# Kernel tuning notes

Hardware: AMD Instinct MI355X
Metric: run time of the kernel (lower is better)

## Reference

```python
import jax, jax.numpy as jnp
import numpy as np

N, E = 50000, 800000
DIN, DH, DOUT = 128, 128, 64


def _w(k, fan_in, fan_out):
    return (jax.random.normal(k, (fan_in, fan_out), jnp.float32) / np.sqrt(fan_in)).astype(jnp.float32)


def setup_inputs() -> dict:
    key = jax.random.key(0)
    ks = jax.random.split(key, 12)
    x = jax.random.normal(ks[0], (N, DIN), jnp.float32)
    edge_index = jax.random.randint(ks[1], (2, E), 0, N, dtype=jnp.int64)
    return {
        "x": x,
        "edge_index": edge_index,
        # sage1 block: SAGEConv(DIN->DH) -> relu -> SAGEConv(DH->DH)
        "Ws11": _w(ks[2], DIN, DH), "Wn11": _w(ks[3], DIN, DH), "b11": jnp.zeros((DH,), jnp.float32),
        "Ws12": _w(ks[4], DH, DH),  "Wn12": _w(ks[5], DH, DH),  "b12": jnp.zeros((DH,), jnp.float32),
        # sage2 block: SAGEConv(DH->DH) -> relu -> SAGEConv(DH->DH)
        "Ws21": _w(ks[6], DH, DH),  "Wn21": _w(ks[7], DH, DH),  "b21": jnp.zeros((DH,), jnp.float32),
        "Ws22": _w(ks[8], DH, DH),  "Wn22": _w(ks[9], DH, DH),  "b22": jnp.zeros((DH,), jnp.float32),
        # classifier
        "Wc": _w(ks[10], DH, DOUT), "bc": jnp.zeros((DOUT,), jnp.float32),
    }


def _sage_conv(h, src, tgt, Ws, Wn, b, n):
    # mean-aggregate neighbor features (src -> tgt), then self + neighbor linear
    msgs = h[src]                                                   # [E, d] gather
    deg = jax.ops.segment_sum(jnp.ones((src.shape[0],), h.dtype), tgt, num_segments=n)
    agg = jax.ops.segment_sum(msgs, tgt, num_segments=n)
    agg = agg / jnp.maximum(deg, 1.0)[:, None]                      # [n, d]
    return h @ Ws + agg @ Wn + b


def reference(x, edge_index, Ws11, Wn11, b11, Ws12, Wn12, b12,
              Ws21, Wn21, b21, Ws22, Wn22, b22, Wc, bc):
    src, tgt = edge_index[0], edge_index[1]
    n = x.shape[0]
    # sage1 block (2 layers) + outer relu
    h = jax.nn.relu(_sage_conv(x, src, tgt, Ws11, Wn11, b11, n))
    h = _sage_conv(h, src, tgt, Ws12, Wn12, b12, n)
    h = jax.nn.relu(h)
    # dropout (eval mode): identity
    # sage2 block (2 layers) + outer relu
    h = jax.nn.relu(_sage_conv(h, src, tgt, Ws21, Wn21, b21, n))
    h = _sage_conv(h, src, tgt, Ws22, Wn22, b22, n)
    h = jax.nn.relu(h)
    # global mean pool over nodes, then classify
    g = jnp.mean(h, axis=0)                                         # [DH]
    return g @ Wc + bc                                              # [DOUT]
```

## Files before the change

kernel.cpp:

```cpp
#include <hip/hip_runtime.h>
#include <hip/hip_bf16.h>
#include <hip/hip_fp16.h>


typedef _Float16 f16x8 __attribute__((ext_vector_type(8)));
typedef float f32x4 __attribute__((ext_vector_type(4)));

__global__ __launch_bounds__(256) void k_bucket(
    const int* __restrict__ src, const int* __restrict__ tgt,
    int* __restrict__ deg, unsigned long long* __restrict__ staging,
    int* __restrict__ bucket_fill, int E, int bdiv, int cap) {
  __shared__ unsigned long long buf[8][320];
  __shared__ int cnt[8];
  __shared__ int base[8];
  int tid = threadIdx.x;
  int lane = tid & 63;
  if (tid < 8) cnt[tid] = 0;
  __syncthreads();
  int e0 = blockIdx.x * 2048;
#pragma unroll
  for (int i = 0; i < 8; ++i) {
    int e = e0 + i * 256 + tid;
    bool valid = e < E;
    int b = -1;
    unsigned long long pair = 0;
    if (valid) {
      int t = tgt[e];
      int s = src[e];
      atomicAdd(&deg[t], 1);
      b = t / bdiv;
      pair = ((unsigned long long)(unsigned)t << 32) | (unsigned)s;
    }
#pragma unroll
    for (int bk = 0; bk < 8; ++bk) {
      bool mine = (b == bk);
      unsigned long long mask = __ballot(mine);
      if (mask == 0ull) continue;
      int cw = __popcll(mask);
      int leader = __ffsll((unsigned long long)mask) - 1;
      int p0 = 0;
      if (lane == leader) p0 = atomicAdd(&cnt[bk], cw);
      p0 = __shfl(p0, leader, 64);
      if (mine) {
        int p = p0 + __popcll(mask & ((1ull << lane) - 1ull));
        if (p < 320) {
          buf[bk][p] = pair;
        } else {
          int gp = atomicAdd(&bucket_fill[bk], 1);
          staging[(size_t)bk * cap + gp] = pair;
        }
      }
    }
  }
  __syncthreads();
  if (tid < 8) {
    int c = min(cnt[tid], 320);
    base[tid] = atomicAdd(&bucket_fill[tid], c);
    cnt[tid] = c;
  }
  __syncthreads();
  for (int b = 0; b < 8; ++b) {
    int c = cnt[b];
    for (int p = tid; p < c; p += 256)
      staging[(size_t)b * cap + base[b] + p] = buf[b][p];
  }
}

__global__ __launch_bounds__(256) void k_scatter2(
    const unsigned long long* __restrict__ staging,
    const int* __restrict__ bucket_fill, int* __restrict__ cursor,
    int* __restrict__ csr_src, int cap) {
  int b = blockIdx.x & 7;
  int nchunk = gridDim.x >> 3;
  int chunk = blockIdx.x >> 3;
  int n = bucket_fill[b];
  const unsigned long long* sb = staging + (size_t)b * cap;
  for (int i0 = chunk * 2048; i0 < n; i0 += nchunk * 2048) {
#pragma unroll
    for (int t = 0; t < 8; ++t) {
      int i = i0 + t * 256 + (int)threadIdx.x;
      if (i < n) {
        unsigned long long pair = sb[i];
        int tg = (int)(pair >> 32);
        int s = (int)(pair & 0xffffffffu);
        int pos = atomicAdd(&cursor[tg], 1);
        csr_src[pos] = s;
      }
    }
  }
}

__global__ __launch_bounds__(256) void k_scan1(const int* __restrict__ deg,
                                               int* __restrict__ partial,
                                               int* __restrict__ blocksum,
                                               float* __restrict__ inv_deg, int n) {
  __shared__ int s[256];
  int tid = threadIdx.x;
  int i = blockIdx.x * 256 + tid;
  int v = (i < n) ? deg[i] : 0;
  s[tid] = v;
  __syncthreads();
  for (int off = 1; off < 256; off <<= 1) {
    int t = (tid >= off) ? s[tid - off] : 0;
    __syncthreads();
    s[tid] += t;
    __syncthreads();
  }
  if (i < n) {
    partial[i] = s[tid] - v;
    inv_deg[i] = 1.0f / fmaxf((float)v, 1.0f);
  }
  if (tid == 255) blocksum[blockIdx.x] = s[255];
}

__global__ __launch_bounds__(256) void k_scan2(int* __restrict__ blocksum, int nb) {
  __shared__ int s[256];
  int tid = threadIdx.x;
  int v = (tid < nb) ? blocksum[tid] : 0;
  s[tid] = v;
  __syncthreads();
  for (int off = 1; off < 256; off <<= 1) {
    int t = (tid >= off) ? s[tid - off] : 0;
    __syncthreads();
    s[tid] += t;
    __syncthreads();
  }
  if (tid < nb) blocksum[tid] = s[tid] - v;
}

__global__ __launch_bounds__(256) void k_scan3(const int* __restrict__ partial,
                                               const int* __restrict__ blocksum,
                                               int* __restrict__ row_start,
                                               int* __restrict__ cursor, int n, int E) {
  int i = blockIdx.x * 256 + threadIdx.x;
  if (i < n) {
    int r = partial[i] + blocksum[blockIdx.x];
    row_start[i] = r;
    cursor[i] = r;
  }
  if (i == 0) row_start[n] = E;
}

__global__ __launch_bounds__(256) void k_cvt_x(const float* __restrict__ x,
                                               __half* __restrict__ xh, int total8) {
  int i = blockIdx.x * 256 + threadIdx.x;
  if (i >= total8) return;
  const float4* p = (const float4*)(x + (size_t)i * 8);
  float4 v0 = p[0], v1 = p[1];
  f16x8 o;
  o[0] = (_Float16)v0.x; o[1] = (_Float16)v0.y; o[2] = (_Float16)v0.z; o[3] = (_Float16)v0.w;
  o[4] = (_Float16)v1.x; o[5] = (_Float16)v1.y; o[6] = (_Float16)v1.z; o[7] = (_Float16)v1.w;
  *(f16x8*)(xh + (size_t)i * 8) = o;
}

struct WPack {
  const float* s[4];
  const float* n[4];
};

__global__ __launch_bounds__(256) void k_prep_w(WPack p, __half* __restrict__ Wt) {
  int l = blockIdx.y;
  int i = blockIdx.x * 256 + threadIdx.x;
  int n = i >> 8;
  int k = i & 255;
  const float* W = (k < 128) ? p.s[l] : p.n[l];
  float v = W[(size_t)(k & 127) * 128 + n];
  Wt[(size_t)l * 32768 + (size_t)n * 256 + k] = __float2half(v);
}

__global__ __launch_bounds__(256) void k_agg_h(
    const __half* __restrict__ h, const int* __restrict__ csr_src,
    const int* __restrict__ row_start, const float* __restrict__ inv_deg,
    __half* __restrict__ agg, int n_nodes) {
  int gw = (blockIdx.x * 256 + (int)threadIdx.x) >> 6;
  int lane = threadIdx.x & 63;
  if (gw >= n_nodes) return;
  int q = lane >> 4;
  int dl = (lane & 15) * 8;
  int beg = row_start[gw];
  int end = row_start[gw + 1];
  float a0 = 0.f, a1 = 0.f, a2 = 0.f, a3 = 0.f;
  float a4 = 0.f, a5 = 0.f, a6 = 0.f, a7 = 0.f;
  int e = beg;
  for (; e + 16 <= end; e += 16) {
    int i0 = csr_src[e + q];
    int i1 = csr_src[e + 4 + q];
    int i2 = csr_src[e + 8 + q];
    int i3 = csr_src[e + 12 + q];
    f16x8 v0 = *(const f16x8*)(h + (size_t)i0 * 128 + dl);
    f16x8 v1 = *(const f16x8*)(h + (size_t)i1 * 128 + dl);
    f16x8 v2 = *(const f16x8*)(h + (size_t)i2 * 128 + dl);
    f16x8 v3 = *(const f16x8*)(h + (size_t)i3 * 128 + dl);
    a0 += ((float)v0[0] + (float)v1[0]) + ((float)v2[0] + (float)v3[0]);
    a1 += ((float)v0[1] + (float)v1[1]) + ((float)v2[1] + (float)v3[1]);
    a2 += ((float)v0[2] + (float)v1[2]) + ((float)v2[2] + (float)v3[2]);
    a3 += ((float)v0[3] + (float)v1[3]) + ((float)v2[3] + (float)v3[3]);
    a4 += ((float)v0[4] + (float)v1[4]) + ((float)v2[4] + (float)v3[4]);
    a5 += ((float)v0[5] + (float)v1[5]) + ((float)v2[5] + (float)v3[5]);
    a6 += ((float)v0[6] + (float)v1[6]) + ((float)v2[6] + (float)v3[6]);
    a7 += ((float)v0[7] + (float)v1[7]) + ((float)v2[7] + (float)v3[7]);
  }
  for (; e + 8 <= end; e += 8) {
    int i0 = csr_src[e + q];
    int i1 = csr_src[e + 4 + q];
    f16x8 v0 = *(const f16x8*)(h + (size_t)i0 * 128 + dl);
    f16x8 v1 = *(const f16x8*)(h + (size_t)i1 * 128 + dl);
    a0 += (float)v0[0] + (float)v1[0];
    a1 += (float)v0[1] + (float)v1[1];
    a2 += (float)v0[2] + (float)v1[2];
    a3 += (float)v0[3] + (float)v1[3];
    a4 += (float)v0[4] + (float)v1[4];
    a5 += (float)v0[5] + (float)v1[5];
    a6 += (float)v0[6] + (float)v1[6];
    a7 += (float)v0[7] + (float)v1[7];
  }
  for (; e + 4 <= end; e += 4) {
    int i0 = csr_src[e + q];
    f16x8 v0 = *(const f16x8*)(h + (size_t)i0 * 128 + dl);
    a0 += (float)v0[0];
    a1 += (float)v0[1];
    a2 += (float)v0[2];
    a3 += (float)v0[3];
    a4 += (float)v0[4];
    a5 += (float)v0[5];
    a6 += (float)v0[6];
    a7 += (float)v0[7];
  }
  if (e + q < end) {
    int i0 = csr_src[e + q];
    f16x8 v0 = *(const f16x8*)(h + (size_t)i0 * 128 + dl);
    a0 += (float)v0[0];
    a1 += (float)v0[1];
    a2 += (float)v0[2];
    a3 += (float)v0[3];
    a4 += (float)v0[4];
    a5 += (float)v0[5];
    a6 += (float)v0[6];
    a7 += (float)v0[7];
  }
  a0 += __shfl_xor(a0, 16, 64);
  a1 += __shfl_xor(a1, 16, 64);
  a2 += __shfl_xor(a2, 16, 64);
  a3 += __shfl_xor(a3, 16, 64);
  a4 += __shfl_xor(a4, 16, 64);
  a5 += __shfl_xor(a5, 16, 64);
  a6 += __shfl_xor(a6, 16, 64);
  a7 += __shfl_xor(a7, 16, 64);
  a0 += __shfl_xor(a0, 32, 64);
  a1 += __shfl_xor(a1, 32, 64);
  a2 += __shfl_xor(a2, 32, 64);
  a3 += __shfl_xor(a3, 32, 64);
  a4 += __shfl_xor(a4, 32, 64);
  a5 += __shfl_xor(a5, 32, 64);
  a6 += __shfl_xor(a6, 32, 64);
  a7 += __shfl_xor(a7, 32, 64);
  if (q == 0) {
    float wgt = inv_deg[gw];
    f16x8 r;
    r[0] = (_Float16)(a0 * wgt);
    r[1] = (_Float16)(a1 * wgt);
    r[2] = (_Float16)(a2 * wgt);
    r[3] = (_Float16)(a3 * wgt);
    r[4] = (_Float16)(a4 * wgt);
    r[5] = (_Float16)(a5 * wgt);
    r[6] = (_Float16)(a6 * wgt);
    r[7] = (_Float16)(a7 * wgt);
    *(f16x8*)(agg + (size_t)gw * 128 + dl) = r;
  }
}

__global__ __launch_bounds__(256) void k_linear_mfma(
    const __half* __restrict__ h, const __half* __restrict__ agg,
    const __half* __restrict__ Wt, const float* __restrict__ bias,
    __half* __restrict__ out, int n_nodes) {
  int tid = threadIdx.x;
  int cq = tid >> 6;
  int lane = tid & 63;
  int node0 = blockIdx.x * 64;
  int lr = lane & 15;
  int lg = lane >> 4;

  f32x4 acc[4][2];
#pragma unroll
  for (int rt = 0; rt < 4; ++rt)
#pragma unroll
    for (int ct = 0; ct < 2; ++ct) acc[rt][ct] = (f32x4){0.f, 0.f, 0.f, 0.f};

  const __half* hrow[4];
  const __half* grow[4];
#pragma unroll
  for (int rt = 0; rt < 4; ++rt) {
    int arow = node0 + rt * 16 + lr;
    if (arow >= n_nodes) arow = n_nodes - 1;
    hrow[rt] = h + (size_t)arow * 128;
    grow[rt] = agg + (size_t)arow * 128;
  }

#pragma unroll
  for (int ks = 0; ks < 8; ++ks) {
    int koff = (ks & 3) * 32 + lg * 8;
    int kb = ks * 32 + lg * 8;
    f16x8 b0 = *(const f16x8*)(Wt + (size_t)(cq * 32 + lr) * 256 + kb);
    f16x8 b1 = *(const f16x8*)(Wt + (size_t)(cq * 32 + 16 + lr) * 256 + kb);
#pragma unroll
    for (int rt = 0; rt < 4; ++rt) {
      f16x8 a = (ks < 4) ? *(const f16x8*)(hrow[rt] + koff)
                         : *(const f16x8*)(grow[rt] + koff);
      acc[rt][0] = __builtin_amdgcn_mfma_f32_16x16x32_f16(a, b0, acc[rt][0], 0, 0, 0);
      acc[rt][1] = __builtin_amdgcn_mfma_f32_16x16x32_f16(a, b1, acc[rt][1], 0, 0, 0);
    }
  }

#pragma unroll
  for (int ct = 0; ct < 2; ++ct) {
    int n_col = cq * 32 + ct * 16 + lr;
    float bv = bias[n_col];
#pragma unroll
    for (int rt = 0; rt < 4; ++rt) {
#pragma unroll
      for (int r = 0; r < 4; ++r) {
        int m = node0 + rt * 16 + lg * 4 + r;
        if (m < n_nodes)
          out[(size_t)m * 128 + n_col] = __float2half(fmaxf(acc[rt][ct][r] + bv, 0.f));
      }
    }
  }
}

__global__ __launch_bounds__(256) void k_pool(const __half* __restrict__ h,
                                              float* __restrict__ partial, int n_nodes) {
  __shared__ float red[4][128];
  int tid = threadIdx.x;
  int lane = tid & 63;
  int w = tid >> 6;
  float a0 = 0.f, a1 = 0.f;
  for (int n = blockIdx.x * 4 + w; n < n_nodes; n += gridDim.x * 4) {
    float2 f = __half22float2(*(const __half2*)(h + (size_t)n * 128 + lane * 2));
    a0 += f.x;
    a1 += f.y;
  }
  red[w][lane * 2] = a0;
  red[w][lane * 2 + 1] = a1;
  __syncthreads();
  if (tid < 128) {
    partial[(size_t)blockIdx.x * 128 + tid] =
        (red[0][tid] + red[1][tid]) + (red[2][tid] + red[3][tid]);
  }
}

__global__ __launch_bounds__(512) void k_final(const float* __restrict__ partial,
                                               const float* __restrict__ Wc,
                                               const float* __restrict__ bc,
                                               float* __restrict__ out, int n_nodes) {
  __shared__ float red[4][128];
  __shared__ float gs[128];
  __shared__ float red2[8][64];
  int tid = threadIdx.x;
  int j = tid & 127;
  int c = tid >> 7;
  float s = 0.f;
#pragma unroll
  for (int b = 0; b < 64; ++b) s += partial[(size_t)(c * 64 + b) * 128 + j];
  red[c][j] = s;
  __syncthreads();
  if (tid < 128) {
    float g = (red[0][tid] + red[1][tid]) + (red[2][tid] + red[3][tid]);
    gs[tid] = g / (float)n_nodes;
  }
  __syncthreads();
  {
    int jo = tid & 63;
    int c2 = tid >> 6;
    float s2 = 0.f;
#pragma unroll
    for (int d = 0; d < 16; ++d)
      s2 += gs[c2 * 16 + d] * Wc[(size_t)(c2 * 16 + d) * 64 + jo];
    red2[c2][jo] = s2;
  }
  __syncthreads();
  if (tid < 64) {
    float o = bc[tid];
#pragma unroll
    for (int c2 = 0; c2 < 8; ++c2) o += red2[c2][tid];
    out[tid] = o;
  }
}

extern "C" void kernel_launch(void* const* d_in, const int* in_sizes, int n_in,
                              void* d_out, int out_size, void* d_ws, size_t ws_size,
                              hipStream_t stream) {
  const float* x = (const float*)d_in[0];
  const int* ei = (const int*)d_in[1];
  const float* Ws11 = (const float*)d_in[2];
  const float* Wn11 = (const float*)d_in[3];
  const float* b11 = (const float*)d_in[4];
  const float* Ws12 = (const float*)d_in[5];
  const float* Wn12 = (const float*)d_in[6];
  const float* b12 = (const float*)d_in[7];
  const float* Ws21 = (const float*)d_in[8];
  const float* Wn21 = (const float*)d_in[9];
  const float* b21 = (const float*)d_in[10];
  const float* Ws22 = (const float*)d_in[11];
  const float* Wn22 = (const float*)d_in[12];
  const float* b22 = (const float*)d_in[13];
  const float* Wc = (const float*)d_in[14];
  const float* bc = (const float*)d_in[15];

  int N = in_sizes[0] / 128;
  int E = in_sizes[1] / 2;
  const int* src = ei;
  const int* tgt = ei + E;

  int bdiv = (N + 7) / 8;
  int cap = E / 8 + 8192;

  char* w = (char*)d_ws;
  size_t off = 0;
  auto alloc = [&](size_t bytes) {
    void* p = w + off;
    off += (bytes + 255) & ~(size_t)255;
    return p;
  };
  __half* xh = (__half*)alloc((size_t)N * 128 * 2);
  __half* hA = (__half*)alloc((size_t)N * 128 * 2);
  __half* hB = (__half*)alloc((size_t)N * 128 * 2);
  __half* aggb = (__half*)alloc((size_t)N * 128 * 2);
  __half* Wt = (__half*)alloc((size_t)4 * 32768 * 2);
  float* partial = (float*)alloc((size_t)256 * 128 * 4);
  float* inv_deg = (float*)alloc((size_t)N * 4);
  int* deg = (int*)alloc((size_t)N * 4);
  int* row_start = (int*)alloc((size_t)(N + 1) * 4);
  int* cursor = (int*)alloc((size_t)N * 4);
  int* csr_src = (int*)alloc((size_t)E * 4);
  int* scanp = (int*)alloc((size_t)N * 4);
  int* blocksum = (int*)alloc((size_t)256 * 4);
  unsigned long long* staging =
      (unsigned long long*)alloc((size_t)8 * cap * 8);
  int* bucket_fill = (int*)alloc((size_t)8 * 4);

  hipMemsetAsync(deg, 0, (size_t)N * 4, stream);
  hipMemsetAsync(bucket_fill, 0, 8 * 4, stream);
  hipMemsetAsync(partial, 0, (size_t)256 * 128 * 4, stream);

  int nb = (N + 255) / 256;
  int bb = (E + 2047) / 2048;
  k_bucket<<<bb, 256, 0, stream>>>(src, tgt, deg, staging, bucket_fill, E, bdiv, cap);
  k_scan1<<<nb, 256, 0, stream>>>(deg, scanp, blocksum, inv_deg, N);
  k_scan2<<<1, 256, 0, stream>>>(blocksum, nb);
  k_scan3<<<nb, 256, 0, stream>>>(scanp, blocksum, row_start, cursor, N, E);
  k_scatter2<<<448, 256, 0, stream>>>(staging, bucket_fill, cursor, csr_src, cap);

  int total8 = N * 128 / 8;
  k_cvt_x<<<(total8 + 255) / 256, 256, 0, stream>>>(x, xh, total8);
  WPack wp;
  wp.s[0] = Ws11; wp.s[1] = Ws12; wp.s[2] = Ws21; wp.s[3] = Ws22;
  wp.n[0] = Wn11; wp.n[1] = Wn12; wp.n[2] = Wn21; wp.n[3] = Wn22;
  k_prep_w<<<dim3(128, 4), 256, 0, stream>>>(wp, Wt);

  int ab = (N + 3) / 4;
  int lb = (N + 63) / 64;

  k_agg_h<<<ab, 256, 0, stream>>>(xh, csr_src, row_start, inv_deg, aggb, N);
  k_linear_mfma<<<lb, 256, 0, stream>>>(xh, aggb, Wt + 0 * 32768, b11, hA, N);
  k_agg_h<<<ab, 256, 0, stream>>>(hA, csr_src, row_start, inv_deg, aggb, N);
  k_linear_mfma<<<lb, 256, 0, stream>>>(hA, aggb, Wt + 1 * 32768, b12, hB, N);
  k_agg_h<<<ab, 256, 0, stream>>>(hB, csr_src, row_start, inv_deg, aggb, N);
  k_linear_mfma<<<lb, 256, 0, stream>>>(hB, aggb, Wt + 2 * 32768, b21, hA, N);
  k_agg_h<<<ab, 256, 0, stream>>>(hA, csr_src, row_start, inv_deg, aggb, N);
  k_linear_mfma<<<lb, 256, 0, stream>>>(hA, aggb, Wt + 3 * 32768, b22, hB, N);

  k_pool<<<256, 256, 0, stream>>>(hB, partial, N);
  k_final<<<1, 512, 0, stream>>>(partial, Wc, bc, (float*)d_out, N);
}
```

Baseline: 348.4 us.

## Split aggregation across feature quarters and move degree counting to LDS histogram

```diff
diff --git a/kernel.cpp b/kernel.cpp
--- a/kernel.cpp
+++ b/kernel.cpp
@@ -8,26 +8,24 @@
 
 __global__ __launch_bounds__(256) void k_bucket(
     const int* __restrict__ src, const int* __restrict__ tgt,
-    int* __restrict__ deg, unsigned long long* __restrict__ staging,
+    unsigned long long* __restrict__ staging,
     int* __restrict__ bucket_fill, int E, int bdiv, int cap) {
-  __shared__ unsigned long long buf[8][320];
+  __shared__ unsigned long long buf[8][96];
   __shared__ int cnt[8];
   __shared__ int base[8];
   int tid = threadIdx.x;
   int lane = tid & 63;
   if (tid < 8) cnt[tid] = 0;
   __syncthreads();
-  int e0 = blockIdx.x * 2048;
-#pragma unroll
-  for (int i = 0; i < 8; ++i) {
+  int e0 = blockIdx.x * 512;
+#pragma unroll
+  for (int i = 0; i < 2; ++i) {
     int e = e0 + i * 256 + tid;
-    bool valid = e < E;
     int b = -1;
     unsigned long long pair = 0;
-    if (valid) {
+    if (e < E) {
       int t = tgt[e];
       int s = src[e];
-      atomicAdd(&deg[t], 1);
       b = t / bdiv;
       pair = ((unsigned long long)(unsigned)t << 32) | (unsigned)s;
     }
@@ -43,7 +41,7 @@
       p0 = __shfl(p0, leader, 64);
       if (mine) {
         int p = p0 + __popcll(mask & ((1ull << lane) - 1ull));
-        if (p < 320) {
+        if (p < 96) {
           buf[bk][p] = pair;
         } else {
           int gp = atomicAdd(&bucket_fill[bk], 1);
@@ -54,15 +52,40 @@
   }
   __syncthreads();
   if (tid < 8) {
-    int c = min(cnt[tid], 320);
+    int c = min(cnt[tid], 96);
     base[tid] = atomicAdd(&bucket_fill[tid], c);
     cnt[tid] = c;
   }
   __syncthreads();
   for (int b = 0; b < 8; ++b) {
     int c = cnt[b];
-    for (int p = tid; p < c; p += 256)
-      staging[(size_t)b * cap + base[b] + p] = buf[b][p];
+    if (tid < c) staging[(size_t)b * cap + base[b] + tid] = buf[b][tid];
+  }
+}
+
+__global__ __launch_bounds__(256) void k_hist(
+    const unsigned long long* __restrict__ staging,
+    const int* __restrict__ bucket_fill, int* __restrict__ deg,
+    int bdiv, int cap, int n) {
+  __shared__ int hist[8192];
+  int tid = threadIdx.x;
+  int bk = blockIdx.x & 7;
+  int sub = blockIdx.x >> 3;
+  int lo = bk * bdiv;
+  int bsize = min(bdiv, n - lo);
+  if (bsize <= 0) return;
+  for (int j = tid; j < bsize; j += 256) hist[j] = 0;
+  __syncthreads();
+  int nb = bucket_fill[bk];
+  const unsigned long long* sb = staging + (size_t)bk * cap;
+  for (int i = sub * 256 + tid; i < nb; i += 8 * 256) {
+    int t = (int)(sb[i] >> 32);
+    atomicAdd(&hist[t - lo], 1);
+  }
+  __syncthreads();
+  for (int j = tid; j < bsize; j += 256) {
+    int v = hist[j];
+    if (v) atomicAdd(&deg[lo + j], v);
   }
 }
 
@@ -172,90 +195,55 @@
     const __half* __restrict__ h, const int* __restrict__ csr_src,
     const int* __restrict__ row_start, const float* __restrict__ inv_deg,
     __half* __restrict__ agg, int n_nodes) {
-  int gw = (blockIdx.x * 256 + (int)threadIdx.x) >> 6;
+  int b = blockIdx.x;
+  int s = b & 3;
+  int node = (b >> 2) * 4 + ((int)threadIdx.x >> 6);
   int lane = threadIdx.x & 63;
-  if (gw >= n_nodes) return;
-  int q = lane >> 4;
-  int dl = (lane & 15) * 8;
-  int beg = row_start[gw];
-  int end = row_start[gw + 1];
+  if (node >= n_nodes) return;
+  int slot = lane >> 2;
+  int doff = s * 32 + (lane & 3) * 8;
+  int beg = row_start[node];
+  int end = row_start[node + 1];
   float a0 = 0.f, a1 = 0.f, a2 = 0.f, a3 = 0.f;
   float a4 = 0.f, a5 = 0.f, a6 = 0.f, a7 = 0.f;
   int e = beg;
   for (; e + 16 <= end; e += 16) {
-    int i0 = csr_src[e + q];
-    int i1 = csr_src[e + 4 + q];
-    int i2 = csr_src[e + 8 + q];
-    int i3 = csr_src[e + 12 + q];
-    f16x8 v0 = *(const f16x8*)(h + (size_t)i0 * 128 + dl);
-    f16x8 v1 = *(const f16x8*)(h + (size_t)i1 * 128 + dl);
-    f16x8 v2 = *(const f16x8*)(h + (size_t)i2 * 128 + dl);
-    f16x8 v3 = *(const f16x8*)(h + (size_t)i3 * 128 + dl);
-    a0 += ((float)v0[0] + (float)v1[0]) + ((float)v2[0] + (float)v3[0]);
-    a1 += ((float)v0[1] + (float)v1[1]) + ((float)v2[1] + (float)v3[1]);
-    a2 += ((float)v0[2] + (float)v1[2]) + ((float)v2[2] + (float)v3[2]);
-    a3 += ((float)v0[3] + (float)v1[3]) + ((float)v2[3] + (float)v3[3]);
-    a4 += ((float)v0[4] + (float)v1[4]) + ((float)v2[4] + (float)v3[4]);
-    a5 += ((float)v0[5] + (float)v1[5]) + ((float)v2[5] + (float)v3[5]);
-    a6 += ((float)v0[6] + (float)v1[6]) + ((float)v2[6] + (float)v3[6]);
-    a7 += ((float)v0[7] + (float)v1[7]) + ((float)v2[7] + (float)v3[7]);
-  }
-  for (; e + 8 <= end; e += 8) {
-    int i0 = csr_src[e + q];
-    int i1 = csr_src[e + 4 + q];
-    f16x8 v0 = *(const f16x8*)(h + (size_t)i0 * 128 + dl);
-    f16x8 v1 = *(const f16x8*)(h + (size_t)i1 * 128 + dl);
-    a0 += (float)v0[0] + (float)v1[0];
-    a1 += (float)v0[1] + (float)v1[1];
-    a2 += (float)v0[2] + (float)v1[2];
-    a3 += (float)v0[3] + (float)v1[3];
-    a4 += (float)v0[4] + (float)v1[4];
-    a5 += (float)v0[5] + (float)v1[5];
-    a6 += (float)v0[6] + (float)v1[6];
-    a7 += (float)v0[7] + (float)v1[7];
-  }
-  for (; e + 4 <= end; e += 4) {
-    int i0 = csr_src[e + q];
-    f16x8 v0 = *(const f16x8*)(h + (size_t)i0 * 128 + dl);
-    a0 += (float)v0[0];
-    a1 += (float)v0[1];
-    a2 += (float)v0[2];
-    a3 += (float)v0[3];
-    a4 += (float)v0[4];
-    a5 += (float)v0[5];
-    a6 += (float)v0[6];
-    a7 += (float)v0[7];
-  }
-  if (e + q < end) {
-    int i0 = csr_src[e + q];
-    f16x8 v0 = *(const f16x8*)(h + (size_t)i0 * 128 + dl);
-    a0 += (float)v0[0];
-    a1 += (float)v0[1];
-    a2 += (float)v0[2];
-    a3 += (float)v0[3];
-    a4 += (float)v0[4];
-    a5 += (float)v0[5];
-    a6 += (float)v0[6];
-    a7 += (float)v0[7];
-  }
-  a0 += __shfl_xor(a0, 16, 64);
-  a1 += __shfl_xor(a1, 16, 64);
-  a2 += __shfl_xor(a2, 16, 64);
-  a3 += __shfl_xor(a3, 16, 64);
-  a4 += __shfl_xor(a4, 16, 64);
-  a5 += __shfl_xor(a5, 16, 64);
-  a6 += __shfl_xor(a6, 16, 64);
-  a7 += __shfl_xor(a7, 16, 64);
-  a0 += __shfl_xor(a0, 32, 64);
-  a1 += __shfl_xor(a1, 32, 64);
-  a2 += __shfl_xor(a2, 32, 64);
-  a3 += __shfl_xor(a3, 32, 64);
-  a4 += __shfl_xor(a4, 32, 64);
-  a5 += __shfl_xor(a5, 32, 64);
-  a6 += __shfl_xor(a6, 32, 64);
-  a7 += __shfl_xor(a7, 32, 64);
-  if (q == 0) {
-    float wgt = inv_deg[gw];
+    int i0 = csr_src[e + slot];
+    f16x8 v = *(const f16x8*)(h + (size_t)i0 * 128 + doff);
+    a0 += (float)v[0];
+    a1 += (float)v[1];
+    a2 += (float)v[2];
+    a3 += (float)v[3];
+    a4 += (float)v[4];
+    a5 += (float)v[5];
+    a6 += (float)v[6];
+    a7 += (float)v[7];
+  }
+  if (e + slot < end) {
+    int i0 = csr_src[e + slot];
+    f16x8 v = *(const f16x8*)(h + (size_t)i0 * 128 + doff);
+    a0 += (float)v[0];
+    a1 += (float)v[1];
+    a2 += (float)v[2];
+    a3 += (float)v[3];
+    a4 += (float)v[4];
+    a5 += (float)v[5];
+    a6 += (float)v[6];
+    a7 += (float)v[7];
+  }
+#pragma unroll
+  for (int off = 4; off <= 32; off <<= 1) {
+    a0 += __shfl_xor(a0, off, 64);
+    a1 += __shfl_xor(a1, off, 64);
+    a2 += __shfl_xor(a2, off, 64);
+    a3 += __shfl_xor(a3, off, 64);
+    a4 += __shfl_xor(a4, off, 64);
+    a5 += __shfl_xor(a5, off, 64);
+    a6 += __shfl_xor(a6, off, 64);
+    a7 += __shfl_xor(a7, off, 64);
+  }
+  if (slot == 0) {
+    float wgt = inv_deg[node];
     f16x8 r;
     r[0] = (_Float16)(a0 * wgt);
     r[1] = (_Float16)(a1 * wgt);
@@ -265,7 +253,7 @@
     r[5] = (_Float16)(a5 * wgt);
     r[6] = (_Float16)(a6 * wgt);
     r[7] = (_Float16)(a7 * wgt);
-    *(f16x8*)(agg + (size_t)gw * 128 + dl) = r;
+    *(f16x8*)(agg + (size_t)node * 128 + doff) = r;
   }
 }
 
@@ -443,8 +431,9 @@
   hipMemsetAsync(partial, 0, (size_t)256 * 128 * 4, stream);
 
   int nb = (N + 255) / 256;
-  int bb = (E + 2047) / 2048;
-  k_bucket<<<bb, 256, 0, stream>>>(src, tgt, deg, staging, bucket_fill, E, bdiv, cap);
+  int bb = (E + 511) / 512;
+  k_bucket<<<bb, 256, 0, stream>>>(src, tgt, staging, bucket_fill, E, bdiv, cap);
+  k_hist<<<64, 256, 0, stream>>>(staging, bucket_fill, deg, bdiv, cap, N);
   k_scan1<<<nb, 256, 0, stream>>>(deg, scanp, blocksum, inv_deg, N);
   k_scan2<<<1, 256, 0, stream>>>(blocksum, nb);
   k_scan3<<<nb, 256, 0, stream>>>(scanp, blocksum, row_start, cursor, N, E);
@@ -457,7 +446,7 @@
   wp.n[0] = Wn11; wp.n[1] = Wn12; wp.n[2] = Wn21; wp.n[3] = Wn22;
   k_prep_w<<<dim3(128, 4), 256, 0, stream>>>(wp, Wt);
 
-  int ab = (N + 3) / 4;
+  int ab = 4 * ((N + 3) / 4);
   int lb = (N + 63) / 64;
 
   k_agg_h<<<ab, 256, 0, stream>>>(xh, csr_src, row_start, inv_deg, aggb, N);
```

New measurement: 519.6 us. +49.2%, slower.
